# Optimization experiments

Measured on AMD Instinct MI355X. Metric: run time of the kernel, lower is better.

## Reference

```python
import jax, jax.numpy as jnp
import numpy as np

B, T, F, H, C = 1024, 64, 256, 1024, 2


def setup_inputs() -> dict:
    key = jax.random.key(0)
    ks = jax.random.split(key, 16)
    s = 1.0 / np.sqrt(H)
    return {
        "X": jax.random.normal(ks[0], (B, T, F), jnp.float32),
        "missing_mask": (jax.random.uniform(ks[1], (B, T, F)) > 0.3).astype(jnp.float32),
        "deltas": jax.random.uniform(ks[2], (B, T, F), jnp.float32) * 5.0,
        "empirical_mean": jax.random.normal(ks[3], (B, F), jnp.float32),
        "X_filledLOCF": jax.random.normal(ks[4], (B, T, F), jnp.float32),
        # TemporalDecay h: full linear F->H
        "w_gh": jax.random.normal(ks[5], (H, F), jnp.float32) * 0.02,
        "b_gh": jnp.zeros((H,), jnp.float32),
        # TemporalDecay x: diagonal (W masked by identity) -> vector of size F
        "w_gx": jax.random.normal(ks[6], (F,), jnp.float32) * 0.02,
        "b_gx": jnp.zeros((F,), jnp.float32),
        # GRUCell: input size 2F+H, hidden H
        "w_ih": jax.random.uniform(ks[7], (3 * H, 2 * F + H), jnp.float32, -s, s),
        "w_hh": jax.random.uniform(ks[8], (3 * H, H), jnp.float32, -s, s),
        "b_ih": jax.random.uniform(ks[9], (3 * H,), jnp.float32, -s, s),
        "b_hh": jax.random.uniform(ks[10], (3 * H,), jnp.float32, -s, s),
        # classifier H -> C
        "w_cls": jax.random.normal(ks[11], (C, H), jnp.float32) * 0.02,
        "b_cls": jnp.zeros((C,), jnp.float32),
    }


def _grud_forward(X, missing_mask, deltas, empirical_mean, X_filledLOCF,
                  w_gh, b_gh, w_gx, b_gx, w_ih, w_hh, b_ih, b_hh, w_cls, b_cls):
    # time-major for scan: [T, B, F]
    Xt = jnp.swapaxes(X, 0, 1)
    Mt = jnp.swapaxes(missing_mask, 0, 1)
    Dt = jnp.swapaxes(deltas, 0, 1)
    Lt = jnp.swapaxes(X_filledLOCF, 0, 1)

    def step(h, xs):
        x, m, d, x_locf = xs
        # TemporalDecay: gamma = exp(-relu(W d + b))
        gamma_h = jnp.exp(-jax.nn.relu(d @ w_gh.T + b_gh))        # [B, H]
        gamma_x = jnp.exp(-jax.nn.relu(d * w_gx + b_gx))          # [B, F] (diag)
        h = h * gamma_h
        x_h = gamma_x * x_locf + (1.0 - gamma_x) * empirical_mean
        x_replaced = m * x + (1.0 - m) * x_h
        inp = jnp.concatenate([x_replaced, h, m], axis=1)         # [B, 2F+H]
        # GRUCell
        gi = inp @ w_ih.T + b_ih                                   # [B, 3H]
        gh = h @ w_hh.T + b_hh                                     # [B, 3H]
        i_r, i_z, i_n = jnp.split(gi, 3, axis=1)
        h_r, h_z, h_n = jnp.split(gh, 3, axis=1)
        r = jax.nn.sigmoid(i_r + h_r)
        z = jax.nn.sigmoid(i_z + h_z)
        n = jnp.tanh(i_n + r * h_n)
        h_new = (1.0 - z) * n + z * h
        return h_new, None

    h0 = jnp.zeros((X.shape[0], w_hh.shape[1]), X.dtype)
    h_final, _ = jax.lax.scan(step, h0, (Xt, Mt, Dt, Lt))
    logits = h_final @ w_cls.T + b_cls
    return jax.nn.softmax(logits, axis=1)


def reference(X, missing_mask, deltas, empirical_mean, X_filledLOCF,
              w_gh, b_gh, w_gx, b_gx, w_ih, w_hh, b_ih, b_hh, w_cls, b_cls):
    return _grud_forward(X, missing_mask, deltas, empirical_mean, X_filledLOCF,
                         w_gh, b_gh, w_gx, b_gx, w_ih, w_hh, b_ih, b_hh, w_cls, b_cls)
```

## Files before the change

kernel.cpp:

```cpp
#include <hip/hip_runtime.h>

using bf16   = __bf16;
using bf16x8 = __bf16 __attribute__((ext_vector_type(8)));
using f32x4  = float  __attribute__((ext_vector_type(4)));


__device__ __forceinline__ float sigm(float x) { return 1.f / (1.f + __expf(-x)); }
__device__ __forceinline__ float tanh_fast(float x) {
  float e = __expf(2.f * x);
  return 1.f - 2.f / (e + 1.f);
}

#define GLL16(gsrc, ldst)                                                              \
  __builtin_amdgcn_global_load_lds((const __attribute__((address_space(1))) void*)(gsrc), \
                                   (__attribute__((address_space(3))) void*)(ldst), 16, 0, 0)

__global__ void prep_kernel(const float* __restrict__ X, const float* __restrict__ Msk,
                            const float* __restrict__ D, const float* __restrict__ Mean,
                            const float* __restrict__ L, const float* __restrict__ w_gx,
                            const float* __restrict__ b_gx,
                            bf16* __restrict__ XRs, bf16* __restrict__ Dbfs,
                            int c, int nsl) {
  int i = blockIdx.x * 256 + threadIdx.x;
  if (i >= (nsl << 18)) return;
  int f = i & 255, b = (i >> 8) & 1023, tl = i >> 18;
  int t = c * 16 + tl;
  size_t g = ((size_t)b << 14) + ((size_t)t << 8) + f;
  float d = D[g];
  int fs = f ^ ((b & 7) << 3);
  int row = tl * 1024 + b;
  Dbfs[(size_t)row * 256 + fs] = (bf16)d;
  float gx = __expf(-fmaxf(d * w_gx[f] + b_gx[f], 0.f));
  float xh = gx * L[g] + (1.f - gx) * Mean[(size_t)b * 256 + f];
  float m  = Msk[g];
  float xr = m * X[g] + (1.f - m) * xh;
  if (tl < 16) {
    size_t xo = (size_t)row * 512;
    XRs[xo + fs]       = (bf16)xr;
    XRs[xo + 256 + fs] = (bf16)m;
  }
}

__global__ void wprep_kernel(const float* __restrict__ w_ih, const float* __restrict__ w_hh,
                             const float* __restrict__ b_ih, const float* __restrict__ b_hh,
                             const float* __restrict__ w_gh,
                             bf16* __restrict__ WcH3, bf16* __restrict__ WcX3,
                             bf16* __restrict__ Wgs, float* __restrict__ bias4) {
  int i = blockIdx.x * 256 + threadIdx.x;
  if (i < 4194304) {
    int blk = i >> 13;
    int nb = blk >> 4, kt = blk & 15;
    int r = i & 8191;
    int nl = r >> 6, cc = (r >> 3) & 7, e = r & 7;
    int gg = nl >> 5, j = nb * 32 + (nl & 31);
    int k = kt * 64 + ((cc ^ (nl & 7)) << 3) + e;
    float v;
    if (gg == 3) v = w_hh[(size_t)(2048 + j) * 1024 + k];
    else {
      int rr = gg * 1024 + j;
      v = w_ih[(size_t)rr * 1536 + 256 + k];
      if (gg < 2) v += w_hh[(size_t)rr * 1024 + k];
    }
    WcH3[i] = (bf16)v;
  } else if (i < 5767168) {
    int q = i - 4194304;
    int blk = q >> 13;
    int nb = blk >> 3, kt = blk & 7;
    int r = q & 8191;
    int nl = r >> 6, cc = (r >> 3) & 7, e = r & 7;
    int gg = nb >> 3;
    int j  = (nb & 7) * 128 + nl;
    int rr = gg * 1024 + j;
    int k = kt * 64 + ((cc ^ (nl & 7)) << 3) + e;
    float v = (k < 256) ? w_ih[(size_t)rr * 1536 + k]
                        : w_ih[(size_t)rr * 1536 + 1280 + (k - 256)];
    WcX3[q] = (bf16)v;
  } else if (i < 6029312) {
    int q = i - 5767168;
    int blk = q >> 13;
    int nb = blk >> 2, kt = blk & 3;
    int r = q & 8191;
    int nl = r >> 6, cc = (r >> 3) & 7, e = r & 7;
    int n = nb * 128 + nl;
    int k = kt * 64 + ((cc ^ (nl & 7)) << 3) + e;
    Wgs[q] = (bf16)w_gh[(size_t)n * 256 + k];
  } else if (i < 6033408) {
    int q = i - 6029312;
    int gg = q >> 10, j = q & 1023;
    float v;
    if (gg == 0)      v = b_ih[j] + b_hh[j];
    else if (gg == 1) v = b_ih[1024 + j] + b_hh[1024 + j];
    else if (gg == 2) v = b_ih[2048 + j];
    else              v = b_hh[2048 + j];
    bias4[q] = v;
  }
}

__global__ __launch_bounds__(256) void gammah_kernel(const bf16* __restrict__ Dbfs,
                                                     const bf16* __restrict__ Wgs,
                                                     const float* __restrict__ b_gh,
                                                     bf16* __restrict__ GH) {
  __shared__ char smem[65536];
  char* As = smem;
  char* Bs = smem + 32768;
  int tid = threadIdx.x, lane = tid & 63, wid = tid >> 6;
  int wr = wid >> 1, wc = wid & 1;
  int cpx = gridDim.x >> 3;
  int wg = (blockIdx.x & 7) * cpx + (blockIdx.x >> 3);
  int nb = wg & 7, mb = wg >> 3;

  const bf16* aA = Dbfs + ((size_t)(mb * 128 + wid * 8 + (lane >> 3))) * 256 + (lane & 7) * 8;
  const bf16* aB = Wgs + (size_t)nb * 4 * 8192 + wid * 512 + lane * 8;

  f32x4 acc[4][4];
#pragma unroll
  for (int a = 0; a < 4; ++a)
#pragma unroll
    for (int b = 0; b < 4; ++b)
#pragma unroll
      for (int q = 0; q < 4; ++q) acc[a][b][q] = 0.f;

#define GM_STAGE(buf, kt)                                                         \
  do {                                                                            \
    _Pragma("unroll")                                                             \
    for (int q = 0; q < 4; ++q)                                                   \
      GLL16(aA + q * (32 * 256) + (kt) * 64, As + (buf) * 16384 + (q * 4 + wid) * 1024); \
    _Pragma("unroll")                                                             \
    for (int q = 0; q < 4; ++q)                                                   \
      GLL16(aB + (size_t)(kt) * 8192 + q * 2048, Bs + (buf) * 16384 + (q * 4 + wid) * 1024); \
  } while (0)

  GM_STAGE(0, 0);
  __syncthreads();
  for (int kt = 0; kt < 4; ++kt) {
    const int cur = kt & 1;
    if (kt < 3) GM_STAGE(cur ^ 1, kt + 1);
#pragma unroll
    for (int kk = 0; kk < 2; ++kk) {
      int kb = kk * 64 + ((lane >> 4) << 4);
      bf16x8 af[4], bfr[4];
#pragma unroll
      for (int mf = 0; mf < 4; ++mf) {
        int row = wr * 64 + mf * 16 + (lane & 15);
        af[mf] = *(const bf16x8*)(As + cur * 16384 + (((row * 128 + kb)) ^ ((row & 7) << 4)));
      }
#pragma unroll
      for (int nf = 0; nf < 4; ++nf) {
        int nl = wc * 64 + nf * 16 + (lane & 15);
        bfr[nf] = *(const bf16x8*)(Bs + cur * 16384 + (((nl * 128 + kb)) ^ ((nl & 7) << 4)));
      }
#pragma unroll
      for (int mf = 0; mf < 4; ++mf)
#pragma unroll
        for (int nf = 0; nf < 4; ++nf)
          acc[mf][nf] = __builtin_amdgcn_mfma_f32_16x16x32_bf16(af[mf], bfr[nf], acc[mf][nf], 0, 0, 0);
    }
    __syncthreads();
  }
  char* ep = smem;
#pragma unroll
  for (int nf = 0; nf < 4; ++nf) {
    int col = wc * 64 + nf * 16 + (lane & 15);
    float bg = b_gh[nb * 128 + col];
#pragma unroll
    for (int mf = 0; mf < 4; ++mf)
#pragma unroll
      for (int reg = 0; reg < 4; ++reg) {
        int row = wr * 64 + mf * 16 + ((lane >> 4) << 2) + reg;
        int cph = ((col >> 3) ^ (((row >> 2) & 3) << 2));
        *(bf16*)(ep + row * 256 + (cph << 4) + (col & 7) * 2) =
            (bf16)__expf(-fmaxf(acc[mf][nf][reg] + bg, 0.f));
      }
  }
  __syncthreads();
#pragma unroll
  for (int p = 0; p < 8; ++p) {
    int idx = p * 256 + tid;
    int row = idx >> 4, c = idx & 15;
    int cph = c ^ (((row >> 2) & 3) << 2);
    bf16x8 v = *(const bf16x8*)(ep + row * 256 + (cph << 4));
    *(bf16x8*)(GH + (size_t)(mb * 128 + row) * 1024 + nb * 128 + c * 8) = v;
  }
}

__global__ __launch_bounds__(256) void gix_kernel(const bf16* __restrict__ XRs,
                                                  const bf16* __restrict__ WcX3,
                                                  bf16* __restrict__ Gi) {
  __shared__ char smem[65536];
  char* As = smem;
  char* Bs = smem + 32768;
  int tid = threadIdx.x, lane = tid & 63, wid = tid >> 6;
  int wr = wid >> 1, wc = wid & 1;
  int cpx = gridDim.x >> 3;
  int wg = (blockIdx.x & 7) * cpx + (blockIdx.x >> 3);
  int nb = wg % 24, mb = wg / 24;

  const bf16* aA = XRs + ((size_t)(mb * 128 + wid * 8 + (lane >> 3))) * 512 + (lane & 7) * 8;
  const bf16* aB = WcX3 + (size_t)nb * 8 * 8192 + wid * 512 + lane * 8;

  f32x4 acc[4][4];
#pragma unroll
  for (int a = 0; a < 4; ++a)
#pragma unroll
    for (int b = 0; b < 4; ++b)
#pragma unroll
      for (int q = 0; q < 4; ++q) acc[a][b][q] = 0.f;

#define GX_STAGE(buf, kt)                                                         \
  do {                                                                            \
    _Pragma("unroll")                                                             \
    for (int q = 0; q < 4; ++q)                                                   \
      GLL16(aA + q * (32 * 512) + (kt) * 64, As + (buf) * 16384 + (q * 4 + wid) * 1024); \
    _Pragma("unroll")                                                             \
    for (int q = 0; q < 4; ++q)                                                   \
      GLL16(aB + (size_t)(kt) * 8192 + q * 2048, Bs + (buf) * 16384 + (q * 4 + wid) * 1024); \
  } while (0)

  GX_STAGE(0, 0);
  __syncthreads();
  for (int kt = 0; kt < 8; ++kt) {
    const int cur = kt & 1;
    if (kt < 7) GX_STAGE(cur ^ 1, kt + 1);
#pragma unroll
    for (int kk = 0; kk < 2; ++kk) {
      int kb = kk * 64 + ((lane >> 4) << 4);
      bf16x8 af[4], bfr[4];
#pragma unroll
      for (int mf = 0; mf < 4; ++mf) {
        int row = wr * 64 + mf * 16 + (lane & 15);
        af[mf] = *(const bf16x8*)(As + cur * 16384 + (((row * 128 + kb)) ^ ((row & 7) << 4)));
      }
#pragma unroll
      for (int nf = 0; nf < 4; ++nf) {
        int nl = wc * 64 + nf * 16 + (lane & 15);
        bfr[nf] = *(const bf16x8*)(Bs + cur * 16384 + (((nl * 128 + kb)) ^ ((nl & 7) << 4)));
      }
#pragma unroll
      for (int mf = 0; mf < 4; ++mf)
#pragma unroll
        for (int nf = 0; nf < 4; ++nf)
          acc[mf][nf] = __builtin_amdgcn_mfma_f32_16x16x32_bf16(af[mf], bfr[nf], acc[mf][nf], 0, 0, 0);
    }
    __syncthreads();
  }
  char* ep = smem;
#pragma unroll
  for (int nf = 0; nf < 4; ++nf) {
    int col = wc * 64 + nf * 16 + (lane & 15);
#pragma unroll
    for (int mf = 0; mf < 4; ++mf)
#pragma unroll
      for (int reg = 0; reg < 4; ++reg) {
        int row = wr * 64 + mf * 16 + ((lane >> 4) << 2) + reg;
        int cph = ((col >> 3) ^ (((row >> 2) & 3) << 2));
        *(bf16*)(ep + row * 256 + (cph << 4) + (col & 7) * 2) = (bf16)acc[mf][nf][reg];
      }
  }
  __syncthreads();
  {
    int sl = mb >> 3, mbl = mb & 7;
    bf16* plane = Gi + (size_t)sl * 3145728 + (size_t)(nb >> 3) * 1048576 + (nb & 7) * 128;
#pragma unroll
    for (int p = 0; p < 8; ++p) {
      int idx = p * 256 + tid;
      int row = idx >> 4, c = idx & 15;
      int cph = c ^ (((row >> 2) & 3) << 2);
      bf16x8 v = *(const bf16x8*)(ep + row * 256 + (cph << 4));
      *(bf16x8*)(plane + (size_t)(mbl * 128 + row) * 1024 + c * 8) = v;
    }
  }
}

__global__ __launch_bounds__(512) void step_kernel(
    const bf16* __restrict__ hbs, const float* __restrict__ hf,
    const bf16* __restrict__ WcH3, const float* __restrict__ bias4,
    const bf16* __restrict__ gi, const bf16* __restrict__ gh_next, int is_last,
    float* __restrict__ hf_next, bf16* __restrict__ hbs_next) {
  __shared__ char smem[49152];
  int tid = threadIdx.x, lane = tid & 63, wid = tid >> 6;
  int wr = wid >> 1, wc = wid & 1;
  int wg = ((blockIdx.x & 7) << 6) + (blockIdx.x >> 3);
  int mb = wg & 15, nb = wg >> 4;

  const bf16* aA = hbs + ((size_t)(mb * 64 + (tid >> 3))) * 1024 + (tid & 7) * 8;
  const bf16* aB = WcH3 + (size_t)nb * 131072 + tid * 8;

  int j = nb * 32 + wc * 16 + (lane & 15);
  bf16  grv[4], gzv[4], gnv[4], ghv[4];
  float hfv[4];
#pragma unroll
  for (int reg = 0; reg < 4; ++reg) {
    int brow = mb * 64 + wr * 16 + ((lane >> 4) << 2) + reg;
    size_t hb_ = (size_t)brow * 1024 + j;
    grv[reg] = gi[hb_];
    gzv[reg] = gi[1048576 + hb_];
    gnv[reg] = gi[2097152 + hb_];
    ghv[reg] = gh_next[hb_];
    hfv[reg] = hf[hb_];
  }

  f32x4 acc[4];
#pragma unroll
  for (int b = 0; b < 4; ++b)
#pragma unroll
    for (int q = 0; q < 4; ++q) acc[b][q] = 0.f;

#define ST_STAGE(buf, kt)                                                         \
  do {                                                                            \
    GLL16(aA + (kt) * 64,                 smem + (buf) * 8192 + wid * 1024);      \
    GLL16(aB + (kt) * 8192,               smem + 16384 + (buf) * 16384 + wid * 1024); \
    GLL16(aB + (kt) * 8192 + 4096,        smem + 16384 + (buf) * 16384 + 8192 + wid * 1024); \
  } while (0)

  ST_STAGE(0, 0);
  __syncthreads();
  for (int kt = 0; kt < 16; ++kt) {
    const int cur = kt & 1;
    if (kt < 15) ST_STAGE(cur ^ 1, kt + 1);
    const char* Ab = smem + cur * 8192;
    const char* Bb = smem + 16384 + cur * 16384;
#pragma unroll
    for (int kk = 0; kk < 2; ++kk) {
      int kb = kk * 64 + ((lane >> 4) << 4);
      int row = wr * 16 + (lane & 15);
      bf16x8 af = *(const bf16x8*)(Ab + (((row * 128 + kb)) ^ ((row & 7) << 4)));
      bf16x8 bfr[4];
#pragma unroll
      for (int g = 0; g < 4; ++g) {
        int nl = g * 32 + wc * 16 + (lane & 15);
        bfr[g] = *(const bf16x8*)(Bb + (((nl * 128 + kb)) ^ ((nl & 7) << 4)));
      }
#pragma unroll
      for (int g = 0; g < 4; ++g)
        acc[g] = __builtin_amdgcn_mfma_f32_16x16x32_bf16(af, bfr[g], acc[g], 0, 0, 0);
    }
    __syncthreads();
  }

  float br = bias4[j], bz = bias4[1024 + j], bn = bias4[2048 + j], bh = bias4[3072 + j];
#pragma unroll
  for (int reg = 0; reg < 4; ++reg) {
    int brow = mb * 64 + wr * 16 + ((lane >> 4) << 2) + reg;
    float pr  = acc[0][reg] + (float)grv[reg] + br;
    float pz  = acc[1][reg] + (float)gzv[reg] + bz;
    float pin = acc[2][reg] + (float)gnv[reg] + bn;
    float phn = acc[3][reg] + bh;
    float r = sigm(pr), z = sigm(pz);
    float nn = tanh_fast(pin + r * phn);
    float hnew = (1.f - z) * nn + z * hfv[reg];
    float gam = is_last ? 1.f : (float)ghv[reg];
    float hd = hnew * gam;
    hf_next[(size_t)brow * 1024 + j] = hd;
    hbs_next[(size_t)brow * 1024 + (j ^ ((brow & 7) << 3))] = (bf16)hd;
  }
}

__global__ void cls_kernel(const float* __restrict__ h, const float* __restrict__ w_cls,
                           const float* __restrict__ b_cls, float* __restrict__ out) {
  int wid = threadIdx.x >> 6, lane = threadIdx.x & 63;
  int b = blockIdx.x * 4 + wid;
  const float* hb = h + (size_t)b * 1024;
  float a0 = 0.f, a1 = 0.f;
#pragma unroll
  for (int e = 0; e < 16; ++e) {
    int i = e * 64 + lane;
    float hv = hb[i];
    a0 += hv * w_cls[i];
    a1 += hv * w_cls[1024 + i];
  }
  for (int off = 32; off; off >>= 1) {
    a0 += __shfl_down(a0, off);
    a1 += __shfl_down(a1, off);
  }
  if (lane == 0) {
    float l0 = a0 + b_cls[0], l1 = a1 + b_cls[1];
    float mx = fmaxf(l0, l1);
    float e0 = __expf(l0 - mx), e1 = __expf(l1 - mx);
    float s = e0 + e1;
    out[b * 2]     = e0 / s;
    out[b * 2 + 1] = e1 / s;
  }
}

extern "C" void kernel_launch(void* const* d_in, const int* in_sizes, int n_in,
                              void* d_out, int out_size, void* d_ws, size_t ws_size,
                              hipStream_t stream) {
  const float* X     = (const float*)d_in[0];
  const float* Msk   = (const float*)d_in[1];
  const float* D     = (const float*)d_in[2];
  const float* Mean  = (const float*)d_in[3];
  const float* L     = (const float*)d_in[4];
  const float* w_gh  = (const float*)d_in[5];
  const float* b_gh  = (const float*)d_in[6];
  const float* w_gx  = (const float*)d_in[7];
  const float* b_gx  = (const float*)d_in[8];
  const float* w_ih  = (const float*)d_in[9];
  const float* w_hh  = (const float*)d_in[10];
  const float* b_ih  = (const float*)d_in[11];
  const float* b_hh  = (const float*)d_in[12];
  const float* w_cls = (const float*)d_in[13];
  const float* b_cls = (const float*)d_in[14];

  char* w = (char*)d_ws;
  bf16*  XRs   = (bf16*)(w);
  bf16*  Dbfs  = (bf16*)(w + 16777216);
  bf16*  GH    = (bf16*)(w + 25690112);
  bf16*  WcX3  = (bf16*)(w + 61341696);
  bf16*  WcH3  = (bf16*)(w + 65536000);
  bf16*  Wgs   = (bf16*)(w + 73924608);
  float* bias4 = (float*)(w + 74448896);
  float* hf0   = (float*)(w + 74465280);
  float* hf1   = (float*)(w + 78659584);
  bf16*  hb0   = (bf16*)(w + 82853888);
  bf16*  hb1   = (bf16*)(w + 84951040);
  bf16*  Gi    = (bf16*)(w + 87048192);

  size_t base = 87048192;
  int GCH = 16;
  while (GCH > 1 && base + (size_t)GCH * 6291456ull > ws_size) GCH >>= 1;

  float* hfp[2] = {hf0, hf1};
  bf16*  hbp[2] = {hb0, hb1};

  hipMemsetAsync(hf0, 0, 4194304, stream);
  hipMemsetAsync(hb0, 0, 2097152, stream);
  wprep_kernel<<<23568, 256, 0, stream>>>(w_ih, w_hh, b_ih, b_hh, w_gh, WcH3, WcX3, Wgs, bias4);

  int t = 0;
  for (int c = 0; c < 4; ++c) {
    int nsl = (c < 3) ? 17 : 16;
    prep_kernel<<<nsl * 1024, 256, 0, stream>>>(X, Msk, D, Mean, L, w_gx, b_gx, XRs, Dbfs, c, nsl);
    gammah_kernel<<<nsl * 64, 256, 0, stream>>>(Dbfs, Wgs, b_gh, GH);
    for (int sub = 0; sub < 16 / GCH; ++sub) {
      gix_kernel<<<GCH * 192, 256, 0, stream>>>(XRs + (size_t)sub * GCH * 524288, WcX3, Gi);
      for (int tl2 = 0; tl2 < GCH; ++tl2, ++t) {
        int tl = sub * GCH + tl2;
        int cur = t & 1, nxt = cur ^ 1;
        step_kernel<<<512, 512, 0, stream>>>(
            hbp[cur], hfp[cur], WcH3, bias4,
            Gi + (size_t)tl2 * 3145728, GH + (size_t)(tl + 1) * 1048576,
            (t == 63) ? 1 : 0, hfp[nxt], hbp[nxt]);
      }
    }
  }
  cls_kernel<<<256, 256, 0, stream>>>(hfp[0], w_cls, b_cls, (float*)d_out);
}
```

Baseline: 1.391 ms.

## Double the batch-row tile in the GRU step kernel to reuse weight fragments

```diff
diff --git a/kernel.cpp b/kernel.cpp
--- a/kernel.cpp
+++ b/kernel.cpp
@@ -276,40 +276,45 @@
     const bf16* __restrict__ WcH3, const float* __restrict__ bias4,
     const bf16* __restrict__ gi, const bf16* __restrict__ gh_next, int is_last,
     float* __restrict__ hf_next, bf16* __restrict__ hbs_next) {
-  __shared__ char smem[49152];
+  __shared__ char smem[65536];
   int tid = threadIdx.x, lane = tid & 63, wid = tid >> 6;
   int wr = wid >> 1, wc = wid & 1;
-  int wg = ((blockIdx.x & 7) << 6) + (blockIdx.x >> 3);
-  int mb = wg & 15, nb = wg >> 4;
-
-  const bf16* aA = hbs + ((size_t)(mb * 64 + (tid >> 3))) * 1024 + (tid & 7) * 8;
+  int wg = ((blockIdx.x & 7) << 5) + (blockIdx.x >> 3);
+  int mb = wg & 7, nb = wg >> 3;
+
+  const bf16* aA = hbs + ((size_t)(mb * 128 + (tid >> 3))) * 1024 + (tid & 7) * 8;
   const bf16* aB = WcH3 + (size_t)nb * 131072 + tid * 8;
 
   int j = nb * 32 + wc * 16 + (lane & 15);
-  bf16  grv[4], gzv[4], gnv[4], ghv[4];
-  float hfv[4];
-#pragma unroll
-  for (int reg = 0; reg < 4; ++reg) {
-    int brow = mb * 64 + wr * 16 + ((lane >> 4) << 2) + reg;
-    size_t hb_ = (size_t)brow * 1024 + j;
-    grv[reg] = gi[hb_];
-    gzv[reg] = gi[1048576 + hb_];
-    gnv[reg] = gi[2097152 + hb_];
-    ghv[reg] = gh_next[hb_];
-    hfv[reg] = hf[hb_];
-  }
-
-  f32x4 acc[4];
-#pragma unroll
-  for (int b = 0; b < 4; ++b)
-#pragma unroll
-    for (int q = 0; q < 4; ++q) acc[b][q] = 0.f;
-
-#define ST_STAGE(buf, kt)                                                         \
-  do {                                                                            \
-    GLL16(aA + (kt) * 64,                 smem + (buf) * 8192 + wid * 1024);      \
-    GLL16(aB + (kt) * 8192,               smem + 16384 + (buf) * 16384 + wid * 1024); \
-    GLL16(aB + (kt) * 8192 + 4096,        smem + 16384 + (buf) * 16384 + 8192 + wid * 1024); \
+  bf16  grv[2][4], gzv[2][4], gnv[2][4], ghv[2][4];
+  float hfv[2][4];
+#pragma unroll
+  for (int mfr = 0; mfr < 2; ++mfr)
+#pragma unroll
+    for (int reg = 0; reg < 4; ++reg) {
+      int brow = mb * 128 + wr * 32 + mfr * 16 + ((lane >> 4) << 2) + reg;
+      size_t hb_ = (size_t)brow * 1024 + j;
+      grv[mfr][reg] = gi[hb_];
+      gzv[mfr][reg] = gi[1048576 + hb_];
+      gnv[mfr][reg] = gi[2097152 + hb_];
+      ghv[mfr][reg] = gh_next[hb_];
+      hfv[mfr][reg] = hf[hb_];
+    }
+
+  f32x4 acc[2][4];
+#pragma unroll
+  for (int a = 0; a < 2; ++a)
+#pragma unroll
+    for (int b = 0; b < 4; ++b)
+#pragma unroll
+      for (int q = 0; q < 4; ++q) acc[a][b][q] = 0.f;
+
+#define ST_STAGE(buf, kt)                                                            \
+  do {                                                                               \
+    GLL16(aA + (kt) * 64,             smem + (buf) * 16384 + wid * 1024);            \
+    GLL16(aA + 65536 + (kt) * 64,     smem + (buf) * 16384 + 8192 + wid * 1024);     \
+    GLL16(aB + (kt) * 8192,           smem + 32768 + (buf) * 16384 + wid * 1024);    \
+    GLL16(aB + (kt) * 8192 + 4096,    smem + 32768 + (buf) * 16384 + 8192 + wid * 1024); \
   } while (0)
 
   ST_STAGE(0, 0);
@@ -317,41 +322,49 @@
   for (int kt = 0; kt < 16; ++kt) {
     const int cur = kt & 1;
     if (kt < 15) ST_STAGE(cur ^ 1, kt + 1);
-    const char* Ab = smem + cur * 8192;
-    const char* Bb = smem + 16384 + cur * 16384;
+    const char* Ab = smem + cur * 16384;
+    const char* Bb = smem + 32768 + cur * 16384;
 #pragma unroll
     for (int kk = 0; kk < 2; ++kk) {
       int kb = kk * 64 + ((lane >> 4) << 4);
-      int row = wr * 16 + (lane & 15);
-      bf16x8 af = *(const bf16x8*)(Ab + (((row * 128 + kb)) ^ ((row & 7) << 4)));
-      bf16x8 bfr[4];
+      bf16x8 af[2], bfr[4];
+#pragma unroll
+      for (int mfr = 0; mfr < 2; ++mfr) {
+        int row = wr * 32 + mfr * 16 + (lane & 15);
+        af[mfr] = *(const bf16x8*)(Ab + (((row * 128 + kb)) ^ ((row & 7) << 4)));
+      }
 #pragma unroll
       for (int g = 0; g < 4; ++g) {
         int nl = g * 32 + wc * 16 + (lane & 15);
         bfr[g] = *(const bf16x8*)(Bb + (((nl * 128 + kb)) ^ ((nl & 7) << 4)));
       }
 #pragma unroll
-      for (int g = 0; g < 4; ++g)
-        acc[g] = __builtin_amdgcn_mfma_f32_16x16x32_bf16(af, bfr[g], acc[g], 0, 0, 0);
+      for (int mfr = 0; mfr < 2; ++mfr)
+#pragma unroll
+        for (int g = 0; g < 4; ++g)
+          acc[mfr][g] = __builtin_amdgcn_mfma_f32_16x16x32_bf16(af[mfr], bfr[g], acc[mfr][g], 0, 0, 0);
     }
     __syncthreads();
   }
 
   float br = bias4[j], bz = bias4[1024 + j], bn = bias4[2048 + j], bh = bias4[3072 + j];
 #pragma unroll
-  for (int reg = 0; reg < 4; ++reg) {
-    int brow = mb * 64 + wr * 16 + ((lane >> 4) << 2) + reg;
-    float pr  = acc[0][reg] + (float)grv[reg] + br;
-    float pz  = acc[1][reg] + (float)gzv[reg] + bz;
-    float pin = acc[2][reg] + (float)gnv[reg] + bn;
-    float phn = acc[3][reg] + bh;
-    float r = sigm(pr), z = sigm(pz);
-    float nn = tanh_fast(pin + r * phn);
-    float hnew = (1.f - z) * nn + z * hfv[reg];
-    float gam = is_last ? 1.f : (float)ghv[reg];
-    float hd = hnew * gam;
-    hf_next[(size_t)brow * 1024 + j] = hd;
-    hbs_next[(size_t)brow * 1024 + (j ^ ((brow & 7) << 3))] = (bf16)hd;
+  for (int mfr = 0; mfr < 2; ++mfr) {
+#pragma unroll
+    for (int reg = 0; reg < 4; ++reg) {
+      int brow = mb * 128 + wr * 32 + mfr * 16 + ((lane >> 4) << 2) + reg;
+      float pr  = acc[mfr][0][reg] + (float)grv[mfr][reg] + br;
+      float pz  = acc[mfr][1][reg] + (float)gzv[mfr][reg] + bz;
+      float pin = acc[mfr][2][reg] + (float)gnv[mfr][reg] + bn;
+      float phn = acc[mfr][3][reg] + bh;
+      float r = sigm(pr), z = sigm(pz);
+      float nn = tanh_fast(pin + r * phn);
+      float hnew = (1.f - z) * nn + z * hfv[mfr][reg];
+      float gam = is_last ? 1.f : (float)ghv[mfr][reg];
+      float hd = hnew * gam;
+      hf_next[(size_t)brow * 1024 + j] = hd;
+      hbs_next[(size_t)brow * 1024 + (j ^ ((brow & 7) << 3))] = (bf16)hd;
+    }
   }
 }
 
@@ -436,7 +449,7 @@
       for (int tl2 = 0; tl2 < GCH; ++tl2, ++t) {
         int tl = sub * GCH + tl2;
         int cur = t & 1, nxt = cur ^ 1;
-        step_kernel<<<512, 512, 0, stream>>>(
+        step_kernel<<<256, 512, 0, stream>>>(
             hbp[cur], hfp[cur], WcH3, bias4,
             Gi + (size_t)tl2 * 3145728, GH + (size_t)(tl + 1) * 1048576,
             (t == 63) ? 1 : 0, hfp[nxt], hbp[nxt]);
```

Measured after the change: 1.452 ms. 4.4% more time.

## Quantize recurrent GEMM to int8 with hi/lo split hidden state

Applied to the files above, without the earlier changes.

```diff
diff --git a/kernel.cpp b/kernel.cpp
--- a/kernel.cpp
+++ b/kernel.cpp
@@ -3,6 +3,7 @@
 using bf16   = __bf16;
 using bf16x8 = __bf16 __attribute__((ext_vector_type(8)));
 using f32x4  = float  __attribute__((ext_vector_type(4)));
+using i32x4  = int    __attribute__((ext_vector_type(4)));
 
 
 __device__ __forceinline__ float sigm(float x) { return 1.f / (1.f + __expf(-x)); }
@@ -44,16 +45,18 @@
 __global__ void wprep_kernel(const float* __restrict__ w_ih, const float* __restrict__ w_hh,
                              const float* __restrict__ b_ih, const float* __restrict__ b_hh,
                              const float* __restrict__ w_gh,
-                             bf16* __restrict__ WcH3, bf16* __restrict__ WcX3,
+                             char* __restrict__ WcH3, bf16* __restrict__ WcX3,
                              bf16* __restrict__ Wgs, float* __restrict__ bias4) {
   int i = blockIdx.x * 256 + threadIdx.x;
   if (i < 4194304) {
-    int blk = i >> 13;
-    int nb = blk >> 4, kt = blk & 15;
-    int r = i & 8191;
-    int nl = r >> 6, cc = (r >> 3) & 7, e = r & 7;
+    int nb = i >> 17;
+    int rem = i & 131071;
+    int kt = rem >> 14;
+    int r2 = rem & 16383;
+    int nl = r2 >> 7, bb = r2 & 127;
+    int cc = bb >> 4, e = bb & 15;
     int gg = nl >> 5, j = nb * 32 + (nl & 31);
-    int k = kt * 64 + ((cc ^ (nl & 7)) << 3) + e;
+    int k = kt * 128 + ((cc ^ (nl & 7)) << 4) + e;
     float v;
     if (gg == 3) v = w_hh[(size_t)(2048 + j) * 1024 + k];
     else {
@@ -61,7 +64,10 @@
       v = w_ih[(size_t)rr * 1536 + 256 + k];
       if (gg < 2) v += w_hh[(size_t)rr * 1024 + k];
     }
-    WcH3[i] = (bf16)v;
+    float sc = (gg >= 2) ? 4096.f : 2048.f;
+    int wq = __float2int_rn(v * sc);
+    wq = wq > 127 ? 127 : (wq < -127 ? -127 : wq);
+    WcH3[i] = (char)wq;
   } else if (i < 5767168) {
     int q = i - 4194304;
     int blk = q >> 13;
@@ -271,19 +277,19 @@
   }
 }
 
-__global__ __launch_bounds__(512) void step_kernel(
-    const bf16* __restrict__ hbs, const float* __restrict__ hf,
-    const bf16* __restrict__ WcH3, const float* __restrict__ bias4,
+__global__ __launch_bounds__(512, 4) void step_kernel(
+    const char* __restrict__ hbs, const float* __restrict__ hf,
+    const char* __restrict__ WcH3, const float* __restrict__ bias4,
     const bf16* __restrict__ gi, const bf16* __restrict__ gh_next, int is_last,
-    float* __restrict__ hf_next, bf16* __restrict__ hbs_next) {
-  __shared__ char smem[49152];
+    float* __restrict__ hf_next, char* __restrict__ hbs_next) {
+  __shared__ char smem[65536];
   int tid = threadIdx.x, lane = tid & 63, wid = tid >> 6;
   int wr = wid >> 1, wc = wid & 1;
   int wg = ((blockIdx.x & 7) << 6) + (blockIdx.x >> 3);
   int mb = wg & 15, nb = wg >> 4;
 
-  const bf16* aA = hbs + ((size_t)(mb * 64 + (tid >> 3))) * 1024 + (tid & 7) * 8;
-  const bf16* aB = WcH3 + (size_t)nb * 131072 + tid * 8;
+  const char* aA = hbs + (size_t)(mb * 64 + (tid >> 3)) * 1024 + (tid & 7) * 16;
+  const char* aB = WcH3 + (size_t)nb * 131072 + (tid >> 3) * 128 + (tid & 7) * 16;
 
   int j = nb * 32 + wc * 16 + (lane & 15);
   bf16  grv[4], gzv[4], gnv[4], ghv[4];
@@ -299,59 +305,76 @@
     hfv[reg] = hf[hb_];
   }
 
-  f32x4 acc[4];
+  i32x4 acch[4], accl[4];
 #pragma unroll
   for (int b = 0; b < 4; ++b)
 #pragma unroll
-    for (int q = 0; q < 4; ++q) acc[b][q] = 0.f;
-
-#define ST_STAGE(buf, kt)                                                         \
-  do {                                                                            \
-    GLL16(aA + (kt) * 64,                 smem + (buf) * 8192 + wid * 1024);      \
-    GLL16(aB + (kt) * 8192,               smem + 16384 + (buf) * 16384 + wid * 1024); \
-    GLL16(aB + (kt) * 8192 + 4096,        smem + 16384 + (buf) * 16384 + 8192 + wid * 1024); \
+    for (int q = 0; q < 4; ++q) { acch[b][q] = 0; accl[b][q] = 0; }
+
+#define ST_STAGE(buf, kt)                                                            \
+  do {                                                                               \
+    GLL16(aA + (kt) * 128,            smem + (buf) * 8192 + wid * 1024);             \
+    GLL16(aA + 1048576 + (kt) * 128,  smem + 16384 + (buf) * 8192 + wid * 1024);     \
+    GLL16(aB + (kt) * 16384,          smem + 32768 + (buf) * 16384 + wid * 1024);    \
+    GLL16(aB + (kt) * 16384 + 8192,   smem + 32768 + (buf) * 16384 + 8192 + wid * 1024); \
   } while (0)
 
   ST_STAGE(0, 0);
   __syncthreads();
-  for (int kt = 0; kt < 16; ++kt) {
+  for (int kt = 0; kt < 8; ++kt) {
     const int cur = kt & 1;
-    if (kt < 15) ST_STAGE(cur ^ 1, kt + 1);
-    const char* Ab = smem + cur * 8192;
-    const char* Bb = smem + 16384 + cur * 16384;
+    if (kt < 7) ST_STAGE(cur ^ 1, kt + 1);
+    const char* Ah = smem + cur * 8192;
+    const char* Al = smem + 16384 + cur * 8192;
+    const char* Bb = smem + 32768 + cur * 16384;
 #pragma unroll
     for (int kk = 0; kk < 2; ++kk) {
       int kb = kk * 64 + ((lane >> 4) << 4);
       int row = wr * 16 + (lane & 15);
-      bf16x8 af = *(const bf16x8*)(Ab + (((row * 128 + kb)) ^ ((row & 7) << 4)));
-      bf16x8 bfr[4];
+      int aoff = row * 128 + (kb ^ ((row & 7) << 4));
+      i32x4 afh = *(const i32x4*)(Ah + aoff);
+      i32x4 afl = *(const i32x4*)(Al + aoff);
+      i32x4 bfr[4];
 #pragma unroll
       for (int g = 0; g < 4; ++g) {
         int nl = g * 32 + wc * 16 + (lane & 15);
-        bfr[g] = *(const bf16x8*)(Bb + (((nl * 128 + kb)) ^ ((nl & 7) << 4)));
-      }
-#pragma unroll
-      for (int g = 0; g < 4; ++g)
-        acc[g] = __builtin_amdgcn_mfma_f32_16x16x32_bf16(af, bfr[g], acc[g], 0, 0, 0);
+        bfr[g] = *(const i32x4*)(Bb + ((nl * 128 + (kb ^ ((nl & 7) << 4)))));
+      }
+#pragma unroll
+      for (int g = 0; g < 4; ++g) {
+        acch[g] = __builtin_amdgcn_mfma_i32_16x16x64_i8(afh, bfr[g], acch[g], 0, 0, 0);
+        accl[g] = __builtin_amdgcn_mfma_i32_16x16x64_i8(afl, bfr[g], accl[g], 0, 0, 0);
+      }
     }
     __syncthreads();
   }
 
+  const float ISCH_RZ = 3.814697265625e-06f;
+  const float ISCL_RZ = 2.9802322387695312e-08f;
+  const float ISCH_N  = 1.9073486328125e-06f;
+  const float ISCL_N  = 1.4901161193847656e-08f;
   float br = bias4[j], bz = bias4[1024 + j], bn = bias4[2048 + j], bh = bias4[3072 + j];
 #pragma unroll
   for (int reg = 0; reg < 4; ++reg) {
     int brow = mb * 64 + wr * 16 + ((lane >> 4) << 2) + reg;
-    float pr  = acc[0][reg] + (float)grv[reg] + br;
-    float pz  = acc[1][reg] + (float)gzv[reg] + bz;
-    float pin = acc[2][reg] + (float)gnv[reg] + bn;
-    float phn = acc[3][reg] + bh;
+    float pr  = (float)acch[0][reg] * ISCH_RZ + (float)accl[0][reg] * ISCL_RZ + (float)grv[reg] + br;
+    float pz  = (float)acch[1][reg] * ISCH_RZ + (float)accl[1][reg] * ISCL_RZ + (float)gzv[reg] + bz;
+    float pin = (float)acch[2][reg] * ISCH_N  + (float)accl[2][reg] * ISCL_N  + (float)gnv[reg] + bn;
+    float phn = (float)acch[3][reg] * ISCH_N  + (float)accl[3][reg] * ISCL_N  + bh;
     float r = sigm(pr), z = sigm(pz);
     float nn = tanh_fast(pin + r * phn);
     float hnew = (1.f - z) * nn + z * hfv[reg];
     float gam = is_last ? 1.f : (float)ghv[reg];
     float hd = hnew * gam;
     hf_next[(size_t)brow * 1024 + j] = hd;
-    hbs_next[(size_t)brow * 1024 + (j ^ ((brow & 7) << 3))] = (bf16)hd;
+    int hi8 = __float2int_rn(hd * 128.f);
+    hi8 = hi8 > 127 ? 127 : (hi8 < -127 ? -127 : hi8);
+    float res = hd - (float)hi8 * 0.0078125f;
+    int lo8 = __float2int_rn(res * 16384.f);
+    lo8 = lo8 > 127 ? 127 : (lo8 < -127 ? -127 : lo8);
+    size_t so = (size_t)brow * 1024 + (j ^ ((brow & 7) << 4));
+    hbs_next[so]           = (char)hi8;
+    hbs_next[so + 1048576] = (char)lo8;
   }
 }
 
@@ -406,13 +429,13 @@
   bf16*  Dbfs  = (bf16*)(w + 16777216);
   bf16*  GH    = (bf16*)(w + 25690112);
   bf16*  WcX3  = (bf16*)(w + 61341696);
-  bf16*  WcH3  = (bf16*)(w + 65536000);
+  char*  WcH3  = (char*)(w + 65536000);
   bf16*  Wgs   = (bf16*)(w + 73924608);
   float* bias4 = (float*)(w + 74448896);
   float* hf0   = (float*)(w + 74465280);
   float* hf1   = (float*)(w + 78659584);
-  bf16*  hb0   = (bf16*)(w + 82853888);
-  bf16*  hb1   = (bf16*)(w + 84951040);
+  char*  hb0   = (char*)(w + 82853888);
+  char*  hb1   = (char*)(w + 84951040);
   bf16*  Gi    = (bf16*)(w + 87048192);
 
   size_t base = 87048192;
@@ -420,7 +443,7 @@
   while (GCH > 1 && base + (size_t)GCH * 6291456ull > ws_size) GCH >>= 1;
 
   float* hfp[2] = {hf0, hf1};
-  bf16*  hbp[2] = {hb0, hb1};
+  char*  hbp[2] = {hb0, hb1};
 
   hipMemsetAsync(hf0, 0, 4194304, stream);
   hipMemsetAsync(hb0, 0, 2097152, stream);
```

Result: faster. 1.292 ms (-7.1%).
